# Optimization experiments

Measured on AMD Instinct MI355X. Metric: run time of the kernel, lower is better.

The kernel has to match this reference:

```python
import jax, jax.numpy as jnp
import numpy as np

N = 100000   # nodes
E = 25000    # hyperedges
M = 640000   # incidence pairs
D = 128      # feature dim (in == out, so no res_linear)
EPS = 1e-5


def setup_inputs() -> dict:
    key = jax.random.key(0)
    ks = jax.random.split(key, 7)
    X = jax.random.normal(ks[0], (N, D), dtype=jnp.float32)
    X0 = jax.random.normal(ks[1], (N, D), dtype=jnp.float32)
    vertex = jax.random.randint(ks[2], (M,), 0, N)
    edges = jax.random.randint(ks[3], (M,), 0, E)
    degE = jax.random.uniform(ks[4], (E, 1), dtype=jnp.float32)
    degV = jax.random.uniform(ks[5], (N, 1), dtype=jnp.float32)
    # xavier-uniform-ish linear weight, no bias
    W = jax.random.normal(ks[6], (D, D), dtype=jnp.float32) * np.float32(1.0 / np.sqrt(D))
    ln_w = jnp.ones((D,), dtype=jnp.float32)
    ln_b = jnp.zeros((D,), dtype=jnp.float32)
    alpha = jnp.asarray(0.1, dtype=jnp.float32)
    beta = jnp.asarray(0.5, dtype=jnp.float32)
    return {"X": X, "X0": X0, "degE": degE, "degV": degV, "W": W,
            "alpha": alpha, "beta": beta, "ln_w": ln_w, "ln_b": ln_b,
            "vertex": vertex, "edges": edges}


def reference(X, X0, degE, degV, W, alpha, beta, ln_w, ln_b, vertex, edges):
    # vertex -> hyperedge aggregation (mean), then degree scale
    Xve = X[vertex]                                          # [M, D]
    esum = jax.ops.segment_sum(Xve, edges, num_segments=E)   # [E, D]
    ecnt = jax.ops.segment_sum(jnp.ones((Xve.shape[0], 1), X.dtype), edges, num_segments=E)
    Xe = (esum / jnp.maximum(ecnt, 1.0)) * degE              # [E, D]
    # hyperedge -> vertex aggregation (sum), degree scale
    Xev = Xe[edges]                                          # [M, D]
    Xv = jax.ops.segment_sum(Xev, vertex, num_segments=N) * degV  # [N, D]
    # residual: in_features == out_features -> residual = Xv itself
    Xh = Xv + Xv
    # LayerNorm over feature dim
    mu = jnp.mean(Xh, axis=-1, keepdims=True)
    var = jnp.mean((Xh - mu) ** 2, axis=-1, keepdims=True)
    Xn = (Xh - mu) * jax.lax.rsqrt(var + EPS) * ln_w + ln_b
    # GCNII combination
    Xi = (1.0 - alpha) * Xn + alpha * X0
    return (1.0 - beta) * Xi + beta * (Xi @ W.T)
```

## Files before the change

kernel.cpp:

```cpp
#include <hip/hip_runtime.h>
#include <hip/hip_fp16.h>
#include <hip/hip_bf16.h>

#define D 128
#define NRR 16
#define NCH 32
#define CVT_BLOCKS 512
#define RE_SL 1600
#define RV_SL 6272

typedef __attribute__((ext_vector_type(8))) short bf16x8;
typedef __attribute__((ext_vector_type(4))) float f32x4;

__device__ __forceinline__ __half2 u2h(unsigned u) { return __builtin_bit_cast(__half2, u); }
__device__ __forceinline__ unsigned pack_h2(float a, float b) {
  __half2 h = __float22half2_rn(make_float2(a, b));
  return __builtin_bit_cast(unsigned, h);
}
__device__ __forceinline__ ushort f2bf(float x) {
  __hip_bfloat16 b = __float2bfloat16(x);
  return __builtin_bit_cast(ushort, b);
}

__global__ __launch_bounds__(512) void count_tab(
    const int* __restrict__ edges, const int* __restrict__ vertex,
    int* __restrict__ T_E, int* __restrict__ T_V, int E, int N, int M,
    const float* __restrict__ X, uint2* __restrict__ Xh,
    const float* __restrict__ X0, uint2* X0h, int do_x0, int xn4) {
  __shared__ int he[RE_SL];
  __shared__ int hv[RV_SL];
  int b = blockIdx.x;
  if (b >= NRR * NCH) {
    const f32x4* X4 = (const f32x4*)X;
    const f32x4* X04 = (const f32x4*)X0;
    int stride = (gridDim.x - NRR * NCH) * 512;
    int lim = do_x0 ? (2 * xn4) : xn4;
    for (int i = (b - NRR * NCH) * 512 + threadIdx.x; i < lim; i += stride) {
      int j = (i < xn4) ? i : (i - xn4);
      f32x4 v = (i < xn4) ? X4[j] : X04[j];
      uint2 o = make_uint2(pack_h2(v[0], v[1]), pack_h2(v[2], v[3]));
      if (i < xn4) Xh[j] = o; else X0h[j] = o;
    }
    return;
  }
  int r = b & (NRR - 1), c = b >> 4;
  int RE = (E + NRR - 1) / NRR, RV = (N + NRR - 1) / NRR;
  int eLo = r * RE, eHi = min(eLo + RE, E);
  int vLo = r * RV, vHi = min(vLo + RV, N);
  int eLen = eHi - eLo, vLen = vHi - vLo;
  for (int i = threadIdx.x; i < eLen; i += 512) he[i] = 0;
  for (int i = threadIdx.x; i < vLen; i += 512) hv[i] = 0;
  __syncthreads();
  const int4* E4 = (const int4*)edges;
  const int4* V4 = (const int4*)vertex;
  int m4 = M >> 2;
  int per = (m4 + NCH - 1) / NCH;
  int i0 = c * per, i1 = min(i0 + per, m4);

#define PROC_CNT(ek, vk)                                               \
  {                                                                    \
    if ((ek).x >= eLo && (ek).x < eHi) atomicAdd(&he[(ek).x - eLo], 1);\
    if ((ek).y >= eLo && (ek).y < eHi) atomicAdd(&he[(ek).y - eLo], 1);\
    if ((ek).z >= eLo && (ek).z < eHi) atomicAdd(&he[(ek).z - eLo], 1);\
    if ((ek).w >= eLo && (ek).w < eHi) atomicAdd(&he[(ek).w - eLo], 1);\
    if ((vk).x >= vLo && (vk).x < vHi) atomicAdd(&hv[(vk).x - vLo], 1);\
    if ((vk).y >= vLo && (vk).y < vHi) atomicAdd(&hv[(vk).y - vLo], 1);\
    if ((vk).z >= vLo && (vk).z < vHi) atomicAdd(&hv[(vk).z - vLo], 1);\
    if ((vk).w >= vLo && (vk).w < vHi) atomicAdd(&hv[(vk).w - vLo], 1);\
  }

  int i = i0 + threadIdx.x;
  for (; i + 1536 < i1; i += 2048) {
    int4 e0 = E4[i], e1 = E4[i + 512], e2 = E4[i + 1024], e3 = E4[i + 1536];
    int4 v0 = V4[i], v1 = V4[i + 512], v2 = V4[i + 1024], v3 = V4[i + 1536];
    PROC_CNT(e0, v0); PROC_CNT(e1, v1); PROC_CNT(e2, v2); PROC_CNT(e3, v3);
  }
  for (; i < i1; i += 512) {
    int4 ek = E4[i];
    int4 vk = V4[i];
    PROC_CNT(ek, vk);
  }
  if (c == NCH - 1) {
    for (int m = (m4 << 2) + threadIdx.x; m < M; m += 512) {
      int e = edges[m], v = vertex[m];
      if (e >= eLo && e < eHi) atomicAdd(&he[e - eLo], 1);
      if (v >= vLo && v < vHi) atomicAdd(&hv[v - vLo], 1);
    }
  }
  __syncthreads();
  for (int i2 = threadIdx.x; i2 < eLen; i2 += 512) T_E[(size_t)c * E + eLo + i2] = he[i2];
  for (int i2 = threadIdx.x; i2 < vLen; i2 += 512) T_V[(size_t)c * N + vLo + i2] = hv[i2];
}

__device__ __forceinline__ int block_exscan(int x, int tid, int* wsum) {
  int lane = tid & 63, w = tid >> 6;
  int v = x;
  #pragma unroll
  for (int off = 1; off < 64; off <<= 1) {
    int t = __shfl_up(v, off);
    if (lane >= off) v += t;
  }
  if (lane == 63) wsum[w] = v;
  __syncthreads();
  if (w == 0 && lane < 16) {
    int s = wsum[lane];
    #pragma unroll
    for (int off = 1; off < 16; off <<= 1) {
      int t = __shfl_up(s, off);
      if (lane >= off) s += t;
    }
    wsum[lane] = s;
  }
  __syncthreads();
  int woff = (w == 0) ? 0 : wsum[w - 1];
  return woff + v - x;
}

__global__ __launch_bounds__(1024) void scan_fused(
    int* __restrict__ T_E, int* __restrict__ C_E, int* __restrict__ A_E, int E,
    int* __restrict__ T_V, int* __restrict__ C_V, int* __restrict__ A_V, int N,
    int* __restrict__ sums, int BE) {
  __shared__ int wsum[16];
  int b = blockIdx.x;
  bool isE = b < BE;
  int* T = isE ? T_E : T_V;
  int* C = isE ? C_E : C_V;
  int* A = isE ? A_E : A_V;
  int len = isE ? E : N;
  int base = (isE ? b : (b - BE)) << 10;
  int id = base + threadIdx.x;
  int run = 0;
  if (id < len) {
    #pragma unroll
    for (int c = 0; c < NCH; ++c) {
      int t = T[(size_t)c * len + id];
      T[(size_t)c * len + id] = run;
      run += t;
    }
    C[id] = run;
  }
  int ex = block_exscan(run, threadIdx.x, wsum);
  if (id < len) A[id] = ex;
  if (threadIdx.x == 0) sums[b] = wsum[15];
}

__global__ __launch_bounds__(1024) void scan_add2(
    int* __restrict__ A_E, int E, int* __restrict__ A_V, int N,
    const int* __restrict__ sums, int BE, int BV,
    const float* __restrict__ W, const float* __restrict__ beta_p,
    ushort* __restrict__ Wbf) {
  int nb = BE + BV;
  if ((int)blockIdx.x >= nb) {
    int idx = (blockIdx.x - nb) * 1024 + threadIdx.x;
    if (idx < D * D) {
      int j = idx >> 7, k = idx & 127;
      float beta = *beta_p;
      float v = beta * W[idx] + ((j == k) ? (1.f - beta) : 0.f);
      Wbf[idx] = f2bf(v);
    }
    return;
  }
  __shared__ int wsum[16];
  __shared__ int pb, pbe;
  int x = ((int)threadIdx.x < nb) ? sums[threadIdx.x] : 0;
  int ex = block_exscan(x, threadIdx.x, wsum);
  if (threadIdx.x == blockIdx.x) pb = ex;
  if ((int)threadIdx.x == BE) pbe = ex;
  __syncthreads();
  bool isE = (int)blockIdx.x < BE;
  int off = isE ? pb : (pb - pbe);
  int* A = isE ? A_E : A_V;
  int len = isE ? E : N;
  int base = (isE ? blockIdx.x : (blockIdx.x - BE)) << 10;
  int i = base + threadIdx.x;
  if (i < len) A[i] += off;
}

__global__ __launch_bounds__(512) void scatter_tab(
    const int* __restrict__ edges, const int* __restrict__ vertex,
    const int* __restrict__ A_E, const int* __restrict__ A_V,
    const int* __restrict__ T_E, const int* __restrict__ T_V,
    int* __restrict__ colE, int* __restrict__ colV, int E, int N, int M) {
  __shared__ int offE[RE_SL];
  __shared__ int curE[RE_SL];
  __shared__ int offV[RV_SL];
  __shared__ int curV[RV_SL];
  int b = blockIdx.x;
  int r = b & (NRR - 1), c = b >> 4;
  int RE = (E + NRR - 1) / NRR, RV = (N + NRR - 1) / NRR;
  int eLo = r * RE, eHi = min(eLo + RE, E);
  int vLo = r * RV, vHi = min(vLo + RV, N);
  int eLen = eHi - eLo, vLen = vHi - vLo;
  for (int i = threadIdx.x; i < eLen; i += 512) {
    offE[i] = A_E[eLo + i] + T_E[(size_t)c * E + eLo + i];
    curE[i] = 0;
  }
  for (int i = threadIdx.x; i < vLen; i += 512) {
    offV[i] = A_V[vLo + i] + T_V[(size_t)c * N + vLo + i];
    curV[i] = 0;
  }
  __syncthreads();
  const int4* E4 = (const int4*)edges;
  const int4* V4 = (const int4*)vertex;
  int m4 = M >> 2;
  int per = (m4 + NCH - 1) / NCH;
  int i0 = c * per, i1 = min(i0 + per, m4);

#define PROC_SCAT(ek, vk)                                                   \
  {                                                                         \
    int es_[4] = {(ek).x, (ek).y, (ek).z, (ek).w};                          \
    int vs_[4] = {(vk).x, (vk).y, (vk).z, (vk).w};                          \
    _Pragma("unroll")                                                       \
    for (int t = 0; t < 4; ++t) {                                           \
      if (es_[t] >= eLo && es_[t] < eHi) {                                  \
        int p2 = atomicAdd(&curE[es_[t] - eLo], 1);                         \
        colE[offE[es_[t] - eLo] + p2] = vs_[t];                             \
      }                                                                     \
      if (vs_[t] >= vLo && vs_[t] < vHi) {                                  \
        int p2 = atomicAdd(&curV[vs_[t] - vLo], 1);                         \
        colV[offV[vs_[t] - vLo] + p2] = es_[t];                             \
      }                                                                     \
    }                                                                       \
  }

  int i = i0 + threadIdx.x;
  for (; i + 512 < i1; i += 1024) {
    int4 ea = E4[i], eb = E4[i + 512];
    int4 va = V4[i], vb = V4[i + 512];
    PROC_SCAT(ea, va);
    PROC_SCAT(eb, vb);
  }
  for (; i < i1; i += 512) {
    int4 ek = E4[i];
    int4 vk = V4[i];
    PROC_SCAT(ek, vk);
  }
  if (c == NCH - 1) {
    for (int m = (m4 << 2) + threadIdx.x; m < M; m += 512) {
      int e = edges[m], v = vertex[m];
      if (e >= eLo && e < eHi) {
        int p = atomicAdd(&curE[e - eLo], 1);
        colE[offE[e - eLo] + p] = v;
      }
      if (v >= vLo && v < vHi) {
        int p = atomicAdd(&curV[v - vLo], 1);
        colV[offV[v - vLo] + p] = e;
      }
    }
  }
}

__global__ __launch_bounds__(256) void edge_agg_q(
    const uint4* __restrict__ Xh4, const float* __restrict__ degE,
    const int* __restrict__ A_E, const int* __restrict__ C_E,
    const int* __restrict__ colE, uint4* __restrict__ Xe4, int E) {
  int ql = threadIdx.x & 15;
  int eid = blockIdx.x * 16 + (threadIdx.x >> 4);
  if (eid >= E) return;
  int s = A_E[eid], cnt = C_E[eid];
  float f0 = 0.f, f1 = 0.f, f2 = 0.f, f3 = 0.f, f4 = 0.f, f5 = 0.f, f6 = 0.f, f7 = 0.f;
  int idx = s, rem = cnt;
  while (rem > 0) {
    int r[16];
    #pragma unroll
    for (int t = 0; t < 16; ++t) r[t] = colE[idx + (t < rem ? t : 0)];
    #pragma unroll
    for (int t = 0; t < 16; ++t) {
      uint4 v = Xh4[(size_t)r[t] * 16 + ql];
      if (t < rem) {
        float2 p0 = __half22float2(u2h(v.x));
        float2 p1 = __half22float2(u2h(v.y));
        float2 p2 = __half22float2(u2h(v.z));
        float2 p3 = __half22float2(u2h(v.w));
        f0 += p0.x; f1 += p0.y; f2 += p1.x; f3 += p1.y;
        f4 += p2.x; f5 += p2.y; f6 += p3.x; f7 += p3.y;
      }
    }
    idx += 16;
    rem -= 16;
  }
  float scale = degE[eid] / fmaxf((float)cnt, 1.0f);
  uint4 o;
  o.x = pack_h2(f0 * scale, f1 * scale);
  o.y = pack_h2(f2 * scale, f3 * scale);
  o.z = pack_h2(f4 * scale, f5 * scale);
  o.w = pack_h2(f6 * scale, f7 * scale);
  Xe4[(size_t)eid * 16 + ql] = o;
}

__global__ __launch_bounds__(256) void vertex_ln_q(
    const uint4* __restrict__ Xe4, const float* __restrict__ X0,
    const uint4* X0h, int useh,
    const float* __restrict__ degV, const float* __restrict__ ln_w,
    const float* __restrict__ ln_b, const float* __restrict__ alpha_p,
    const int* __restrict__ A_V, const int* __restrict__ C_V,
    const int* __restrict__ colV, uint4* __restrict__ Xi4, int N) {
  int ql = threadIdx.x & 15;
  int n = blockIdx.x * 16 + (threadIdx.x >> 4);
  if (n >= N) return;
  int s = A_V[n], cnt = C_V[n];
  float f0 = 0.f, f1 = 0.f, f2 = 0.f, f3 = 0.f, f4 = 0.f, f5 = 0.f, f6 = 0.f, f7 = 0.f;
  int idx = s, rem = cnt;
  while (rem > 0) {
    int r[8];
    #pragma unroll
    for (int t = 0; t < 8; ++t) r[t] = colV[idx + (t < rem ? t : 0)];
    #pragma unroll
    for (int t = 0; t < 8; ++t) {
      uint4 v = Xe4[(size_t)r[t] * 16 + ql];
      if (t < rem) {
        float2 p0 = __half22float2(u2h(v.x));
        float2 p1 = __half22float2(u2h(v.y));
        float2 p2 = __half22float2(u2h(v.z));
        float2 p3 = __half22float2(u2h(v.w));
        f0 += p0.x; f1 += p0.y; f2 += p1.x; f3 += p1.y;
        f4 += p2.x; f5 += p2.y; f6 += p3.x; f7 += p3.y;
      }
    }
    idx += 8;
    rem -= 8;
  }
  float sm = ((f0 + f1) + (f2 + f3)) + ((f4 + f5) + (f6 + f7));
  float qq = ((f0 * f0 + f1 * f1) + (f2 * f2 + f3 * f3)) +
             ((f4 * f4 + f5 * f5) + (f6 * f6 + f7 * f7));
  #pragma unroll
  for (int off = 1; off < 16; off <<= 1) {
    sm += __shfl_xor(sm, off);
    qq += __shfl_xor(qq, off);
  }
  float dv = degV[n];
  float csc = 2.f * dv;
  float mu = csc * sm * (1.f / 128.f);
  float var = csc * csc * qq * (1.f / 128.f) - mu * mu;
  float rstd = rsqrtf(var + 1e-5f);
  float x00[8];
  if (useh) {
    uint4 xh = X0h[(size_t)n * 16 + ql];
    float2 q0 = __half22float2(u2h(xh.x));
    float2 q1 = __half22float2(u2h(xh.y));
    float2 q2 = __half22float2(u2h(xh.z));
    float2 q3 = __half22float2(u2h(xh.w));
    x00[0] = q0.x; x00[1] = q0.y; x00[2] = q1.x; x00[3] = q1.y;
    x00[4] = q2.x; x00[5] = q2.y; x00[6] = q3.x; x00[7] = q3.y;
  } else {
    f32x4 x0a = ((const f32x4*)X0)[(size_t)n * 32 + ql * 2];
    f32x4 x0b = ((const f32x4*)X0)[(size_t)n * 32 + ql * 2 + 1];
    x00[0] = x0a[0]; x00[1] = x0a[1]; x00[2] = x0a[2]; x00[3] = x0a[3];
    x00[4] = x0b[0]; x00[5] = x0b[1]; x00[6] = x0b[2]; x00[7] = x0b[3];
  }
  const f32x4* lw4 = (const f32x4*)ln_w;
  const f32x4* lb4 = (const f32x4*)ln_b;
  f32x4 lwa = lw4[ql * 2], lwb = lw4[ql * 2 + 1];
  f32x4 lba = lb4[ql * 2], lbb = lb4[ql * 2 + 1];
  float alpha = *alpha_p;
  float ff[8] = {f0, f1, f2, f3, f4, f5, f6, f7};
  float lww[8] = {lwa[0], lwa[1], lwa[2], lwa[3], lwb[0], lwb[1], lwb[2], lwb[3]};
  float lbs[8] = {lba[0], lba[1], lba[2], lba[3], lbb[0], lbb[1], lbb[2], lbb[3]};
  ushort ob[8];
  #pragma unroll
  for (int i = 0; i < 8; ++i) {
    float xh = csc * ff[i];
    float xn = (xh - mu) * rstd * lww[i] + lbs[i];
    float xi = (1.f - alpha) * xn + alpha * x00[i];
    ob[i] = f2bf(xi);
  }
  uint4 o;
  o.x = (unsigned)ob[0] | ((unsigned)ob[1] << 16);
  o.y = (unsigned)ob[2] | ((unsigned)ob[3] << 16);
  o.z = (unsigned)ob[4] | ((unsigned)ob[5] << 16);
  o.w = (unsigned)ob[6] | ((unsigned)ob[7] << 16);
  Xi4[(size_t)n * 16 + ql] = o;
}

__global__ __launch_bounds__(256) void gemm_out(
    const ushort* __restrict__ Xi_bf, const ushort* __restrict__ Wbf,
    float* __restrict__ out, int N) {
  __shared__ __align__(16) ushort Wl[128 * 128];
  for (int t = threadIdx.x; t < 2048; t += 256) {
    int j = t >> 4, chunk = t & 15;
    bf16x8 v = ((const bf16x8*)Wbf)[t];
    ((bf16x8*)Wl)[j * 16 + (chunk ^ (j & 7))] = v;
  }
  __syncthreads();
  int wv = threadIdx.x >> 6, lane = threadIdx.x & 63;
  int row0 = blockIdx.x * 128 + wv * 32;
  f32x4 acc[2][8] = {};
  #pragma unroll
  for (int ks = 0; ks < 4; ++ks) {
    bf16x8 a[2];
    #pragma unroll
    for (int rt = 0; rt < 2; ++rt) {
      int row = row0 + rt * 16 + (lane & 15);
      row = row < N ? row : N - 1;
      a[rt] = *(const bf16x8*)(Xi_bf + (size_t)row * 128 + ks * 32 + (lane >> 4) * 8);
    }
    int chunk = ks * 4 + (lane >> 4);
    #pragma unroll
    for (int c = 0; c < 8; ++c) {
      int col = c * 16 + (lane & 15);
      bf16x8 bb = ((const bf16x8*)Wl)[col * 16 + (chunk ^ (col & 7))];
      acc[0][c] = __builtin_amdgcn_mfma_f32_16x16x32_bf16(a[0], bb, acc[0][c], 0, 0, 0);
      acc[1][c] = __builtin_amdgcn_mfma_f32_16x16x32_bf16(a[1], bb, acc[1][c], 0, 0, 0);
    }
  }
  #pragma unroll
  for (int rt = 0; rt < 2; ++rt) {
    #pragma unroll
    for (int c = 0; c < 8; ++c) {
      #pragma unroll
      for (int i = 0; i < 4; ++i) {
        int row = row0 + rt * 16 + (lane >> 4) * 4 + i;
        int col = c * 16 + (lane & 15);
        if (row < N) out[(size_t)row * 128 + col] = acc[rt][c][i];
      }
    }
  }
}

extern "C" void kernel_launch(void* const* d_in, const int* in_sizes, int n_in,
                              void* d_out, int out_size, void* d_ws, size_t ws_size,
                              hipStream_t stream) {
  const float* X     = (const float*)d_in[0];
  const float* X0    = (const float*)d_in[1];
  const float* degE  = (const float*)d_in[2];
  const float* degV  = (const float*)d_in[3];
  const float* W     = (const float*)d_in[4];
  const float* alpha = (const float*)d_in[5];
  const float* beta  = (const float*)d_in[6];
  const float* lnw   = (const float*)d_in[7];
  const float* lnb   = (const float*)d_in[8];
  const int* vertex  = (const int*)d_in[9];
  const int* edges   = (const int*)d_in[10];

  const int N = in_sizes[0] / D;
  const int E = in_sizes[2];
  const int M = in_sizes[9];

  const int BE = (E + 1023) >> 10;
  const int BV = (N + 1023) >> 10;

  char* p = (char*)d_ws;
  auto alloc = [&](size_t bytes) { char* r = p; p += (bytes + 255) & ~255ull; return r; };
  int* A_E  = (int*)alloc((size_t)E * 4);
  int* A_V  = (int*)alloc((size_t)N * 4);
  int* C_E  = (int*)alloc((size_t)E * 4);
  int* C_V  = (int*)alloc((size_t)N * 4);
  int* sums = (int*)alloc(1024);
  int* colE = (int*)alloc((size_t)M * 4);
  int* colV = (int*)alloc((size_t)M * 4);
  int* T_E  = (int*)alloc((size_t)NCH * E * 4);
  int* T_V  = (int*)alloc((size_t)NCH * N * 4);
  uint2* X_h  = (uint2*)alloc((size_t)N * D * 2);
  uint4* Xe4  = (uint4*)alloc((size_t)E * D * 2);
  ushort* Wbf = (ushort*)alloc(16384 * 2);
  uint4* Xi4  = (uint4*)X_h;

  size_t used = (size_t)(p - (char*)d_ws);
  size_t x0h_bytes = ((size_t)N * D * 2 + 255) & ~255ull;
  int do_x0 = (used + x0h_bytes <= ws_size) ? 1 : 0;
  uint2* X0h = do_x0 ? (uint2*)alloc((size_t)N * D * 2) : nullptr;

  count_tab<<<NRR * NCH + CVT_BLOCKS, 512, 0, stream>>>(
      edges, vertex, T_E, T_V, E, N, M, X, X_h, X0, X0h, do_x0, N * D / 4);
  scan_fused<<<BE + BV, 1024, 0, stream>>>(T_E, C_E, A_E, E, T_V, C_V, A_V, N, sums, BE);
  scan_add2<<<BE + BV + 16, 1024, 0, stream>>>(A_E, E, A_V, N, sums, BE, BV, W, beta, Wbf);
  scatter_tab<<<NRR * NCH, 512, 0, stream>>>(edges, vertex, A_E, A_V, T_E, T_V,
                                             colE, colV, E, N, M);
  edge_agg_q<<<(E + 15) / 16, 256, 0, stream>>>((const uint4*)X_h, degE, A_E, C_E,
                                                colE, Xe4, E);
  vertex_ln_q<<<(N + 15) / 16, 256, 0, stream>>>(Xe4, X0, (const uint4*)X0h, do_x0,
                                                 degV, lnw, lnb, alpha,
                                                 A_V, C_V, colV, Xi4, N);
  gemm_out<<<(N + 127) / 128, 256, 0, stream>>>((const ushort*)Xi4, Wbf, (float*)d_out, N);
}
```

Measured before the change: 138.2 us.

## Fuse vertex aggregation/LayerNorm with output GEMM via shared-memory Xi tile

Merges the vertex gather+LayerNorm kernel and the bf16 MFMA GEMM into one kernel. Each block computes 64 rows of Xi into LDS (padded stride 136) and multiplies them by W held in LDS, so the Xi round trip through global memory and one launch are gone. In exchange, each block reloads the 32KB W into LDS for only 64 rows instead of 128, and LDS use rises to about 49KB per block, which may reduce occupancy for the latency-bound gather.

After: 165.8 us. +20.0%, slower.

```diff
diff --git a/kernel.cpp b/kernel.cpp
--- a/kernel.cpp
+++ b/kernel.cpp
@@ -288,131 +288,127 @@
   Xe4[(size_t)eid * 16 + ql] = o;
 }
 
-__global__ __launch_bounds__(256) void vertex_ln_q(
+__global__ __launch_bounds__(256) void vertex_fused(
     const uint4* __restrict__ Xe4, const float* __restrict__ X0,
     const uint4* X0h, int useh,
     const float* __restrict__ degV, const float* __restrict__ ln_w,
     const float* __restrict__ ln_b, const float* __restrict__ alpha_p,
     const int* __restrict__ A_V, const int* __restrict__ C_V,
-    const int* __restrict__ colV, uint4* __restrict__ Xi4, int N) {
+    const int* __restrict__ colV, const ushort* __restrict__ Wbf,
+    float* __restrict__ out, int N) {
+  __shared__ __align__(16) ushort Wl[128 * 128];
+  __shared__ __align__(16) ushort XiT[64 * 136];
+  for (int t = threadIdx.x; t < 2048; t += 256) {
+    int j = t >> 4, chunk = t & 15;
+    bf16x8 v = ((const bf16x8*)Wbf)[t];
+    ((bf16x8*)Wl)[j * 16 + (chunk ^ (j & 7))] = v;
+  }
   int ql = threadIdx.x & 15;
-  int n = blockIdx.x * 16 + (threadIdx.x >> 4);
-  if (n >= N) return;
-  int s = A_V[n], cnt = C_V[n];
-  float f0 = 0.f, f1 = 0.f, f2 = 0.f, f3 = 0.f, f4 = 0.f, f5 = 0.f, f6 = 0.f, f7 = 0.f;
-  int idx = s, rem = cnt;
-  while (rem > 0) {
-    int r[8];
-    #pragma unroll
-    for (int t = 0; t < 8; ++t) r[t] = colV[idx + (t < rem ? t : 0)];
-    #pragma unroll
-    for (int t = 0; t < 8; ++t) {
-      uint4 v = Xe4[(size_t)r[t] * 16 + ql];
-      if (t < rem) {
-        float2 p0 = __half22float2(u2h(v.x));
-        float2 p1 = __half22float2(u2h(v.y));
-        float2 p2 = __half22float2(u2h(v.z));
-        float2 p3 = __half22float2(u2h(v.w));
-        f0 += p0.x; f1 += p0.y; f2 += p1.x; f3 += p1.y;
-        f4 += p2.x; f5 += p2.y; f6 += p3.x; f7 += p3.y;
-      }
-    }
-    idx += 8;
-    rem -= 8;
-  }
-  float sm = ((f0 + f1) + (f2 + f3)) + ((f4 + f5) + (f6 + f7));
-  float qq = ((f0 * f0 + f1 * f1) + (f2 * f2 + f3 * f3)) +
-             ((f4 * f4 + f5 * f5) + (f6 * f6 + f7 * f7));
-  #pragma unroll
-  for (int off = 1; off < 16; off <<= 1) {
-    sm += __shfl_xor(sm, off);
-    qq += __shfl_xor(qq, off);
-  }
-  float dv = degV[n];
-  float csc = 2.f * dv;
-  float mu = csc * sm * (1.f / 128.f);
-  float var = csc * csc * qq * (1.f / 128.f) - mu * mu;
-  float rstd = rsqrtf(var + 1e-5f);
-  float x00[8];
-  if (useh) {
-    uint4 xh = X0h[(size_t)n * 16 + ql];
-    float2 q0 = __half22float2(u2h(xh.x));
-    float2 q1 = __half22float2(u2h(xh.y));
-    float2 q2 = __half22float2(u2h(xh.z));
-    float2 q3 = __half22float2(u2h(xh.w));
-    x00[0] = q0.x; x00[1] = q0.y; x00[2] = q1.x; x00[3] = q1.y;
-    x00[4] = q2.x; x00[5] = q2.y; x00[6] = q3.x; x00[7] = q3.y;
-  } else {
-    f32x4 x0a = ((const f32x4*)X0)[(size_t)n * 32 + ql * 2];
-    f32x4 x0b = ((const f32x4*)X0)[(size_t)n * 32 + ql * 2 + 1];
-    x00[0] = x0a[0]; x00[1] = x0a[1]; x00[2] = x0a[2]; x00[3] = x0a[3];
-    x00[4] = x0b[0]; x00[5] = x0b[1]; x00[6] = x0b[2]; x00[7] = x0b[3];
-  }
+  int grp = threadIdx.x >> 4;
+  int n0 = blockIdx.x * 64;
   const f32x4* lw4 = (const f32x4*)ln_w;
   const f32x4* lb4 = (const f32x4*)ln_b;
   f32x4 lwa = lw4[ql * 2], lwb = lw4[ql * 2 + 1];
   f32x4 lba = lb4[ql * 2], lbb = lb4[ql * 2 + 1];
   float alpha = *alpha_p;
-  float ff[8] = {f0, f1, f2, f3, f4, f5, f6, f7};
-  float lww[8] = {lwa[0], lwa[1], lwa[2], lwa[3], lwb[0], lwb[1], lwb[2], lwb[3]};
-  float lbs[8] = {lba[0], lba[1], lba[2], lba[3], lbb[0], lbb[1], lbb[2], lbb[3]};
-  ushort ob[8];
-  #pragma unroll
-  for (int i = 0; i < 8; ++i) {
-    float xh = csc * ff[i];
-    float xn = (xh - mu) * rstd * lww[i] + lbs[i];
-    float xi = (1.f - alpha) * xn + alpha * x00[i];
-    ob[i] = f2bf(xi);
-  }
-  uint4 o;
-  o.x = (unsigned)ob[0] | ((unsigned)ob[1] << 16);
-  o.y = (unsigned)ob[2] | ((unsigned)ob[3] << 16);
-  o.z = (unsigned)ob[4] | ((unsigned)ob[5] << 16);
-  o.w = (unsigned)ob[6] | ((unsigned)ob[7] << 16);
-  Xi4[(size_t)n * 16 + ql] = o;
-}
-
-__global__ __launch_bounds__(256) void gemm_out(
-    const ushort* __restrict__ Xi_bf, const ushort* __restrict__ Wbf,
-    float* __restrict__ out, int N) {
-  __shared__ __align__(16) ushort Wl[128 * 128];
-  for (int t = threadIdx.x; t < 2048; t += 256) {
-    int j = t >> 4, chunk = t & 15;
-    bf16x8 v = ((const bf16x8*)Wbf)[t];
-    ((bf16x8*)Wl)[j * 16 + (chunk ^ (j & 7))] = v;
-  }
-  __syncthreads();
+
+  #pragma unroll 1
+  for (int p = 0; p < 4; ++p) {
+    int r = p * 16 + grp;
+    int n = n0 + r;
+    uint4 o = make_uint4(0u, 0u, 0u, 0u);
+    if (n < N) {
+      int s = A_V[n], cnt = C_V[n];
+      float f0 = 0.f, f1 = 0.f, f2 = 0.f, f3 = 0.f, f4 = 0.f, f5 = 0.f, f6 = 0.f, f7 = 0.f;
+      int idx = s, rem = cnt;
+      while (rem > 0) {
+        int rr[8];
+        #pragma unroll
+        for (int t = 0; t < 8; ++t) rr[t] = colV[idx + (t < rem ? t : 0)];
+        #pragma unroll
+        for (int t = 0; t < 8; ++t) {
+          uint4 v = Xe4[(size_t)rr[t] * 16 + ql];
+          if (t < rem) {
+            float2 p0 = __half22float2(u2h(v.x));
+            float2 p1 = __half22float2(u2h(v.y));
+            float2 p2 = __half22float2(u2h(v.z));
+            float2 p3 = __half22float2(u2h(v.w));
+            f0 += p0.x; f1 += p0.y; f2 += p1.x; f3 += p1.y;
+            f4 += p2.x; f5 += p2.y; f6 += p3.x; f7 += p3.y;
+          }
+        }
+        idx += 8;
+        rem -= 8;
+      }
+      float sm = ((f0 + f1) + (f2 + f3)) + ((f4 + f5) + (f6 + f7));
+      float qq = ((f0 * f0 + f1 * f1) + (f2 * f2 + f3 * f3)) +
+                 ((f4 * f4 + f5 * f5) + (f6 * f6 + f7 * f7));
+      #pragma unroll
+      for (int off = 1; off < 16; off <<= 1) {
+        sm += __shfl_xor(sm, off);
+        qq += __shfl_xor(qq, off);
+      }
+      float dv = degV[n];
+      float csc = 2.f * dv;
+      float mu = csc * sm * (1.f / 128.f);
+      float var = csc * csc * qq * (1.f / 128.f) - mu * mu;
+      float rstd = rsqrtf(var + 1e-5f);
+      float x00[8];
+      if (useh) {
+        uint4 xh = X0h[(size_t)n * 16 + ql];
+        float2 q0 = __half22float2(u2h(xh.x));
+        float2 q1 = __half22float2(u2h(xh.y));
+        float2 q2 = __half22float2(u2h(xh.z));
+        float2 q3 = __half22float2(u2h(xh.w));
+        x00[0] = q0.x; x00[1] = q0.y; x00[2] = q1.x; x00[3] = q1.y;
+        x00[4] = q2.x; x00[5] = q2.y; x00[6] = q3.x; x00[7] = q3.y;
+      } else {
+        f32x4 x0a = ((const f32x4*)X0)[(size_t)n * 32 + ql * 2];
+        f32x4 x0b = ((const f32x4*)X0)[(size_t)n * 32 + ql * 2 + 1];
+        x00[0] = x0a[0]; x00[1] = x0a[1]; x00[2] = x0a[2]; x00[3] = x0a[3];
+        x00[4] = x0b[0]; x00[5] = x0b[1]; x00[6] = x0b[2]; x00[7] = x0b[3];
+      }
+      float ff[8] = {f0, f1, f2, f3, f4, f5, f6, f7};
+      float lww[8] = {lwa[0], lwa[1], lwa[2], lwa[3], lwb[0], lwb[1], lwb[2], lwb[3]};
+      float lbs[8] = {lba[0], lba[1], lba[2], lba[3], lbb[0], lbb[1], lbb[2], lbb[3]};
+      ushort ob[8];
+      #pragma unroll
+      for (int i = 0; i < 8; ++i) {
+        float xhv = csc * ff[i];
+        float xn = (xhv - mu) * rstd * lww[i] + lbs[i];
+        float xi = (1.f - alpha) * xn + alpha * x00[i];
+        ob[i] = f2bf(xi);
+      }
+      o.x = (unsigned)ob[0] | ((unsigned)ob[1] << 16);
+      o.y = (unsigned)ob[2] | ((unsigned)ob[3] << 16);
+      o.z = (unsigned)ob[4] | ((unsigned)ob[5] << 16);
+      o.w = (unsigned)ob[6] | ((unsigned)ob[7] << 16);
+    }
+    *(uint4*)(&XiT[r * 136 + ql * 8]) = o;
+  }
+  __syncthreads();
+
   int wv = threadIdx.x >> 6, lane = threadIdx.x & 63;
-  int row0 = blockIdx.x * 128 + wv * 32;
-  f32x4 acc[2][8] = {};
+  f32x4 acc[8] = {};
   #pragma unroll
   for (int ks = 0; ks < 4; ++ks) {
-    bf16x8 a[2];
-    #pragma unroll
-    for (int rt = 0; rt < 2; ++rt) {
-      int row = row0 + rt * 16 + (lane & 15);
-      row = row < N ? row : N - 1;
-      a[rt] = *(const bf16x8*)(Xi_bf + (size_t)row * 128 + ks * 32 + (lane >> 4) * 8);
-    }
-    int chunk = ks * 4 + (lane >> 4);
+    int row = wv * 16 + (lane & 15);
+    int slot = ks * 4 + (lane >> 4);
+    bf16x8 a = *(const bf16x8*)(&XiT[row * 136 + slot * 8]);
     #pragma unroll
     for (int c = 0; c < 8; ++c) {
       int col = c * 16 + (lane & 15);
-      bf16x8 bb = ((const bf16x8*)Wl)[col * 16 + (chunk ^ (col & 7))];
-      acc[0][c] = __builtin_amdgcn_mfma_f32_16x16x32_bf16(a[0], bb, acc[0][c], 0, 0, 0);
-      acc[1][c] = __builtin_amdgcn_mfma_f32_16x16x32_bf16(a[1], bb, acc[1][c], 0, 0, 0);
+      bf16x8 bb = ((const bf16x8*)Wl)[col * 16 + (slot ^ (col & 7))];
+      acc[c] = __builtin_amdgcn_mfma_f32_16x16x32_bf16(a, bb, acc[c], 0, 0, 0);
     }
   }
   #pragma unroll
-  for (int rt = 0; rt < 2; ++rt) {
-    #pragma unroll
-    for (int c = 0; c < 8; ++c) {
-      #pragma unroll
-      for (int i = 0; i < 4; ++i) {
-        int row = row0 + rt * 16 + (lane >> 4) * 4 + i;
-        int col = c * 16 + (lane & 15);
-        if (row < N) out[(size_t)row * 128 + col] = acc[rt][c][i];
-      }
+  for (int c = 0; c < 8; ++c) {
+    #pragma unroll
+    for (int i = 0; i < 4; ++i) {
+      int row = n0 + wv * 16 + (lane >> 4) * 4 + i;
+      int col = c * 16 + (lane & 15);
+      if (row < N) out[(size_t)row * 128 + col] = acc[c][i];
     }
   }
 }
@@ -453,7 +449,6 @@
   uint2* X_h  = (uint2*)alloc((size_t)N * D * 2);
   uint4* Xe4  = (uint4*)alloc((size_t)E * D * 2);
   ushort* Wbf = (ushort*)alloc(16384 * 2);
-  uint4* Xi4  = (uint4*)X_h;
 
   size_t used = (size_t)(p - (char*)d_ws);
   size_t x0h_bytes = ((size_t)N * D * 2 + 255) & ~255ull;
@@ -468,8 +463,7 @@
                                              colE, colV, E, N, M);
   edge_agg_q<<<(E + 15) / 16, 256, 0, stream>>>((const uint4*)X_h, degE, A_E, C_E,
                                                 colE, Xe4, E);
-  vertex_ln_q<<<(N + 15) / 16, 256, 0, stream>>>(Xe4, X0, (const uint4*)X0h, do_x0,
-                                                 degV, lnw, lnb, alpha,
-                                                 A_V, C_V, colV, Xi4, N);
-  gemm_out<<<(N + 127) / 128, 256, 0, stream>>>((const ushort*)Xi4, Wbf, (float*)d_out, N);
-}
+  vertex_fused<<<(N + 63) / 64, 256, 0, stream>>>(
+      Xe4, X0, (const uint4*)X0h, do_x0, degV, lnw, lnb, alpha,
+      A_V, C_V, colV, Wbf, (float*)d_out, N);
+}
```

## Split histogram counting into separate edge and vertex blocks with coarser partitions

Applied to the files above, without the earlier changes.

The counting kernel now gives each block a single key array (edges or vertices) with its own range split: 4 ranges for edges, 8 for vertices, held in one shared histogram. Before, every block scanned both key arrays for a 16-way range split. This cuts redundant global reads of the incidence arrays. The chunk count drops from 32 to 16, so each count and scatter block processes twice as many pairs. That leaves fewer blocks, fewer partial tables and less scan work, at the cost of less parallelism and larger shared-memory histograms per block, which may lower occupancy.

Result: no change. 137.4 us (-0.6%).

```diff
diff --git a/kernel.cpp b/kernel.cpp
--- a/kernel.cpp
+++ b/kernel.cpp
@@ -3,8 +3,13 @@
 #include <hip/hip_bf16.h>
 
 #define D 128
-#define NRR 16
-#define NCH 32
+#define NCH 16
+#define NRE 4
+#define NRV 8
+#define E_BLKS (NRE * NCH)
+#define V_BLKS (NRV * NCH)
+#define H_SL 12544
+#define SNR 16
 #define CVT_BLOCKS 512
 #define RE_SL 1600
 #define RV_SL 6272
@@ -27,15 +32,14 @@
     int* __restrict__ T_E, int* __restrict__ T_V, int E, int N, int M,
     const float* __restrict__ X, uint2* __restrict__ Xh,
     const float* __restrict__ X0, uint2* X0h, int do_x0, int xn4) {
-  __shared__ int he[RE_SL];
-  __shared__ int hv[RV_SL];
+  __shared__ int h[H_SL];
   int b = blockIdx.x;
-  if (b >= NRR * NCH) {
+  if (b >= E_BLKS + V_BLKS) {
     const f32x4* X4 = (const f32x4*)X;
     const f32x4* X04 = (const f32x4*)X0;
-    int stride = (gridDim.x - NRR * NCH) * 512;
+    int stride = (gridDim.x - E_BLKS - V_BLKS) * 512;
     int lim = do_x0 ? (2 * xn4) : xn4;
-    for (int i = (b - NRR * NCH) * 512 + threadIdx.x; i < lim; i += stride) {
+    for (int i = (b - E_BLKS - V_BLKS) * 512 + threadIdx.x; i < lim; i += stride) {
       int j = (i < xn4) ? i : (i - xn4);
       f32x4 v = (i < xn4) ? X4[j] : X04[j];
       uint2 o = make_uint2(pack_h2(v[0], v[1]), pack_h2(v[2], v[3]));
@@ -43,53 +47,50 @@
     }
     return;
   }
-  int r = b & (NRR - 1), c = b >> 4;
-  int RE = (E + NRR - 1) / NRR, RV = (N + NRR - 1) / NRR;
-  int eLo = r * RE, eHi = min(eLo + RE, E);
-  int vLo = r * RV, vHi = min(vLo + RV, N);
-  int eLen = eHi - eLo, vLen = vHi - vLo;
-  for (int i = threadIdx.x; i < eLen; i += 512) he[i] = 0;
-  for (int i = threadIdx.x; i < vLen; i += 512) hv[i] = 0;
-  __syncthreads();
-  const int4* E4 = (const int4*)edges;
-  const int4* V4 = (const int4*)vertex;
+  const int* keys; int* T; int lo, hi, c, total;
+  if (b < E_BLKS) {
+    int r = b & (NRE - 1); c = b >> 2;
+    int R = (E + NRE - 1) / NRE;
+    lo = r * R; hi = min(lo + R, E); keys = edges; T = T_E; total = E;
+  } else {
+    int bb = b - E_BLKS;
+    int r = bb & (NRV - 1); c = bb >> 3;
+    int R = (N + NRV - 1) / NRV;
+    lo = r * R; hi = min(lo + R, N); keys = vertex; T = T_V; total = N;
+  }
+  int len = hi - lo;
+  for (int i = threadIdx.x; i < len; i += 512) h[i] = 0;
+  __syncthreads();
+  const int4* K4 = (const int4*)keys;
   int m4 = M >> 2;
   int per = (m4 + NCH - 1) / NCH;
   int i0 = c * per, i1 = min(i0 + per, m4);
 
-#define PROC_CNT(ek, vk)                                               \
+#define PROC1(k)                                                       \
   {                                                                    \
-    if ((ek).x >= eLo && (ek).x < eHi) atomicAdd(&he[(ek).x - eLo], 1);\
-    if ((ek).y >= eLo && (ek).y < eHi) atomicAdd(&he[(ek).y - eLo], 1);\
-    if ((ek).z >= eLo && (ek).z < eHi) atomicAdd(&he[(ek).z - eLo], 1);\
-    if ((ek).w >= eLo && (ek).w < eHi) atomicAdd(&he[(ek).w - eLo], 1);\
-    if ((vk).x >= vLo && (vk).x < vHi) atomicAdd(&hv[(vk).x - vLo], 1);\
-    if ((vk).y >= vLo && (vk).y < vHi) atomicAdd(&hv[(vk).y - vLo], 1);\
-    if ((vk).z >= vLo && (vk).z < vHi) atomicAdd(&hv[(vk).z - vLo], 1);\
-    if ((vk).w >= vLo && (vk).w < vHi) atomicAdd(&hv[(vk).w - vLo], 1);\
+    if ((k).x >= lo && (k).x < hi) atomicAdd(&h[(k).x - lo], 1);       \
+    if ((k).y >= lo && (k).y < hi) atomicAdd(&h[(k).y - lo], 1);       \
+    if ((k).z >= lo && (k).z < hi) atomicAdd(&h[(k).z - lo], 1);       \
+    if ((k).w >= lo && (k).w < hi) atomicAdd(&h[(k).w - lo], 1);       \
   }
 
   int i = i0 + threadIdx.x;
   for (; i + 1536 < i1; i += 2048) {
-    int4 e0 = E4[i], e1 = E4[i + 512], e2 = E4[i + 1024], e3 = E4[i + 1536];
-    int4 v0 = V4[i], v1 = V4[i + 512], v2 = V4[i + 1024], v3 = V4[i + 1536];
-    PROC_CNT(e0, v0); PROC_CNT(e1, v1); PROC_CNT(e2, v2); PROC_CNT(e3, v3);
+    int4 k0 = K4[i], k1 = K4[i + 512], k2 = K4[i + 1024], k3 = K4[i + 1536];
+    PROC1(k0); PROC1(k1); PROC1(k2); PROC1(k3);
   }
   for (; i < i1; i += 512) {
-    int4 ek = E4[i];
-    int4 vk = V4[i];
-    PROC_CNT(ek, vk);
+    int4 k = K4[i];
+    PROC1(k);
   }
   if (c == NCH - 1) {
     for (int m = (m4 << 2) + threadIdx.x; m < M; m += 512) {
-      int e = edges[m], v = vertex[m];
-      if (e >= eLo && e < eHi) atomicAdd(&he[e - eLo], 1);
-      if (v >= vLo && v < vHi) atomicAdd(&hv[v - vLo], 1);
-    }
-  }
-  __syncthreads();
-  for (int i2 = threadIdx.x; i2 < eLen; i2 += 512) T_E[(size_t)c * E + eLo + i2] = he[i2];
-  for (int i2 = threadIdx.x; i2 < vLen; i2 += 512) T_V[(size_t)c * N + vLo + i2] = hv[i2];
+      int k = keys[m];
+      if (k >= lo && k < hi) atomicAdd(&h[k - lo], 1);
+    }
+  }
+  __syncthreads();
+  for (int i2 = threadIdx.x; i2 < len; i2 += 512) T[(size_t)c * total + lo + i2] = h[i2];
 }
 
 __device__ __forceinline__ int block_exscan(int x, int tid, int* wsum) {
@@ -186,8 +187,8 @@
   __shared__ int offV[RV_SL];
   __shared__ int curV[RV_SL];
   int b = blockIdx.x;
-  int r = b & (NRR - 1), c = b >> 4;
-  int RE = (E + NRR - 1) / NRR, RV = (N + NRR - 1) / NRR;
+  int r = b & (SNR - 1), c = b >> 4;
+  int RE = (E + SNR - 1) / SNR, RV = (N + SNR - 1) / SNR;
   int eLo = r * RE, eHi = min(eLo + RE, E);
   int vLo = r * RV, vHi = min(vLo + RV, N);
   int eLen = eHi - eLo, vLen = vHi - vLo;
@@ -460,11 +461,11 @@
   int do_x0 = (used + x0h_bytes <= ws_size) ? 1 : 0;
   uint2* X0h = do_x0 ? (uint2*)alloc((size_t)N * D * 2) : nullptr;
 
-  count_tab<<<NRR * NCH + CVT_BLOCKS, 512, 0, stream>>>(
+  count_tab<<<E_BLKS + V_BLKS + CVT_BLOCKS, 512, 0, stream>>>(
       edges, vertex, T_E, T_V, E, N, M, X, X_h, X0, X0h, do_x0, N * D / 4);
   scan_fused<<<BE + BV, 1024, 0, stream>>>(T_E, C_E, A_E, E, T_V, C_V, A_V, N, sums, BE);
   scan_add2<<<BE + BV + 16, 1024, 0, stream>>>(A_E, E, A_V, N, sums, BE, BV, W, beta, Wbf);
-  scatter_tab<<<NRR * NCH, 512, 0, stream>>>(edges, vertex, A_E, A_V, T_E, T_V,
+  scatter_tab<<<SNR * NCH, 512, 0, stream>>>(edges, vertex, A_E, A_V, T_E, T_V,
                                              colE, colV, E, N, M);
   edge_agg_q<<<(E + 15) / 16, 256, 0, stream>>>((const uint4*)X_h, degE, A_E, C_E,
                                                 colE, Xe4, E);
```
